# Optimization experiments

Hardware: AMD Instinct MI355X
Metric: run time of the kernel (lower is better)

## Reference

```python
import jax, jax.numpy as jnp
import numpy as np

NL, DM, DI, DS, DC, DR, NC = 4, 128, 256, 16, 4, 8, 10
ALPHA = 0.3  # observer_alpha

def layernorm(x, w, b, eps=1e-5):
    m = x.mean(-1, keepdims=True)
    v = ((x - m) ** 2).mean(-1, keepdims=True)
    return (x - m) / jnp.sqrt(v + eps) * w + b

def silu(x):
    return x * jax.nn.sigmoid(x)

def causal_dwconv(x, w, b):
    # x: (B, L, DI); w: (DI, 1, DC); b: (DI,)
    xt = x.transpose(0, 2, 1)  # (B, DI, L)
    y = jax.lax.conv_general_dilated(
        xt, w, window_strides=(1,), padding=[(DC - 1, 0)],
        dimension_numbers=('NCH', 'OIH', 'NCH'), feature_group_count=DI)
    return (y + b[None, :, None]).transpose(0, 2, 1)  # (B, L, DI)

def ssm_scan(delta, Bc, Cc, u, A):
    # delta, u: (B, L, DI); Bc, Cc: (B, L, DS); A: (DI, DS)
    B = delta.shape[0]
    def step(h, inp):
        d_t, b_t, c_t, u_t = inp  # (B,DI),(B,DS),(B,DS),(B,DI)
        dA = jnp.exp(d_t[..., None] * A)              # (B, DI, DS)
        h = dA * h + (d_t * u_t)[..., None] * b_t[:, None, :]
        y = jnp.einsum('bds,bs->bd', h, c_t)
        return h, y
    h0 = jnp.zeros((B, DI, DS), delta.dtype)
    xs = (delta.transpose(1, 0, 2), Bc.transpose(1, 0, 2),
          Cc.transpose(1, 0, 2), u.transpose(1, 0, 2))
    _, ys = jax.lax.scan(step, h0, xs)
    return ys.transpose(1, 0, 2)  # (B, L, DI)

def _forward(x, W_in, b_in, ln_w, ln_b, in_proj_w, conv_w, conv_b, x_proj_w,
             dt_proj_w, dt_proj_b, A_log, Dp, out_proj_w, out_proj_b,
             norm_w, norm_b, cls_w, cls_b):
    B = x.shape[0]
    u = x.transpose(0, 2, 3, 1).reshape(B, -1, 3)   # (B, L, 3)
    h = u @ W_in + b_in                              # (B, L, DM)
    for i in range(NL):
        res = h
        z = layernorm(h, ln_w[i], ln_b[i])
        xz = z @ in_proj_w[i]                        # (B, L, 2*DI)
        xin, gate = jnp.split(xz, 2, axis=-1)
        xc = silu(causal_dwconv(xin, conv_w[i], conv_b[i]))  # (B, L, DI)
        proj = xc @ x_proj_w[i]                      # (B, L, DR + 2*DS)
        dt, Bc, Cc = jnp.split(proj, [DR, DR + DS], axis=-1)
        delta = jax.nn.softplus(dt @ dt_proj_w[i] + dt_proj_b[i])  # (B, L, DI)
        A = -jnp.exp(A_log[i])                       # (DI, DS)
        y = ssm_scan(delta, Bc, Cc, xc, A) + xc * Dp[i]
        # Luenberger-style observer correction: blend predicted SSM output
        y = (1.0 - ALPHA) * y + ALPHA * xc
        y = y * silu(gate)
        h = res + y @ out_proj_w[i] + out_proj_b[i]
    pooled = h.mean(axis=1)                          # (B, DM)
    pooled = layernorm(pooled, norm_w, norm_b)
    return pooled @ cls_w + cls_b                    # (B, NC)

def setup_inputs():
    key = jax.random.key(0)
    ks = jax.random.split(key, 8)
    def nrm(k, shape, std=0.02):
        return jax.random.normal(k, shape, jnp.float32) * std
    return {
        'x': jax.random.normal(ks[0], (32, 3, 32, 32), jnp.float32),
        'W_in': nrm(ks[1], (3, DM)), 'b_in': jnp.zeros((DM,), jnp.float32),
        'ln_w': jnp.ones((NL, DM), jnp.float32), 'ln_b': jnp.zeros((NL, DM), jnp.float32),
        'in_proj_w': nrm(ks[2], (NL, DM, 2 * DI)),
        'conv_w': nrm(ks[3], (NL, DI, 1, DC), 0.2), 'conv_b': jnp.zeros((NL, DI), jnp.float32),
        'x_proj_w': nrm(ks[4], (NL, DI, DR + 2 * DS)),
        'dt_proj_w': nrm(ks[5], (NL, DR, DI), 0.1),
        'dt_proj_b': jnp.full((NL, DI), -4.6, jnp.float32),
        'A_log': jnp.log(jnp.broadcast_to(jnp.arange(1, DS + 1, dtype=jnp.float32), (NL, DI, DS))),
        'Dp': jnp.ones((NL, DI), jnp.float32),
        'out_proj_w': nrm(ks[6], (NL, DI, DM)), 'out_proj_b': jnp.zeros((NL, DM), jnp.float32),
        'norm_w': jnp.ones((DM,), jnp.float32), 'norm_b': jnp.zeros((DM,), jnp.float32),
        'cls_w': nrm(ks[7], (DM, NC)), 'cls_b': jnp.zeros((NC,), jnp.float32),
    }

def reference(x, W_in, b_in, ln_w, ln_b, in_proj_w, conv_w, conv_b, x_proj_w,
              dt_proj_w, dt_proj_b, A_log, Dp, out_proj_w, out_proj_b,
              norm_w, norm_b, cls_w, cls_b):
    return _forward(x, W_in, b_in, ln_w, ln_b, in_proj_w, conv_w, conv_b,
                    x_proj_w, dt_proj_w, dt_proj_b, A_log, Dp, out_proj_w,
                    out_proj_b, norm_w, norm_b, cls_w, cls_b)
```

## Files before the change

### kernel.cpp

```cpp
#include <hip/hip_runtime.h>
#include <math.h>

#define B_  32
#define L_  1024
#define T_  (B_ * L_)
#define DM_ 128
#define DI_ 256
#define DS_ 16
#define DC_ 4
#define DR_ 8
#define NC_ 10
#define CHUNK_ 32
#define NCH_  (L_ / CHUNK_)
#define PSTR_ 64

typedef __bf16 bf16x8 __attribute__((ext_vector_type(8)));
typedef __bf16 bf16x4 __attribute__((ext_vector_type(4)));
typedef __bf16 bf16x2 __attribute__((ext_vector_type(2)));
typedef float f32x4 __attribute__((ext_vector_type(4)));

__device__ __forceinline__ float sigmoidf_(float x) { return 1.0f / (1.0f + __expf(-x)); }
__device__ __forceinline__ float siluf_(float x)    { return x * sigmoidf_(x); }
__device__ __forceinline__ float softplusf_(float x) {
    return (x > 15.0f) ? x : __logf(1.0f + __expf(x));
}
__device__ __forceinline__ float fexp2_(float x) { return __builtin_amdgcn_exp2f(x); }

__device__ __forceinline__ void gload_lds16(const __bf16* g, __bf16* l) {
    __builtin_amdgcn_global_load_lds(
        (const __attribute__((address_space(1))) void*)g,
        (__attribute__((address_space(3))) void*)l, 16, 0, 0);
}

template<int R>
__device__ __forceinline__ void stage_async(const __bf16* __restrict__ src,
        __bf16* lds, int k0, int stride, int wid, int lane) {
    constexpr int NI = R / 32;
#pragma unroll
    for (int j = 0; j < NI; ++j) {
        int s0 = (wid * NI + j) * 64;
        int s = s0 + lane;
        int row = s >> 3, sw = s & 7;
        int slot = sw ^ (row & 7);
        gload_lds16(src + (size_t)row * stride + k0 + slot * 8, lds + (size_t)s0 * 8);
    }
}

__global__ __launch_bounds__(128) void k_embed(const float* __restrict__ x,
        const float* __restrict__ Win, const float* __restrict__ bin,
        float* __restrict__ h) {
    int t = blockIdx.x;
    int b = t >> 10, l = t & 1023;
    int m = threadIdx.x;
    const float* xb = x + (size_t)b * 3 * 1024 + l;
    float acc = bin[m];
    acc = fmaf(xb[0],    Win[m],        acc);
    acc = fmaf(xb[1024], Win[128 + m],  acc);
    acc = fmaf(xb[2048], Win[256 + m],  acc);
    h[(size_t)t * 128 + m] = acc;
}

__global__ __launch_bounds__(256) void k_prep(const float* __restrict__ ipw,
        const float* __restrict__ opw, const float* __restrict__ xpw,
        __bf16* __restrict__ wt1, __bf16* __restrict__ wt2,
        __bf16* __restrict__ wcat) {
    int blk = blockIdx.x;
    int tid = threadIdx.x;
    int i = blk * 256 + tid;
    {
        int lay = i >> 16, rem = i & 65535, n = rem >> 7, k = rem & 127;
        wt1[i] = (__bf16)ipw[lay * 65536 + k * 512 + n];
    }
    if (i < 131072) {
        int lay = i >> 15, rem = i & 32767, n = rem >> 8, k = rem & 255;
        wt2[i] = (__bf16)opw[lay * 32768 + k * 128 + n];
    }
    if (blk < 256) {
        int lay = blk >> 6, n = blk & 63;
        int k = tid;
        float v = (n < 40) ? xpw[lay * 10240 + k * 40 + n] : 0.0f;
        wcat[(size_t)blk * 256 + k] = (__bf16)v;
    }
}

__global__ __launch_bounds__(256) void k_ln(const float* __restrict__ h,
        const float* __restrict__ w, const float* __restrict__ b,
        __bf16* __restrict__ z) {
    int wid = threadIdx.x >> 6, lane = threadIdx.x & 63;
    int t = blockIdx.x * 4 + wid;
    const float* hr = h + (size_t)t * 128;
    float2 v = *(const float2*)(hr + lane * 2);
    float s = v.x + v.y, sq = v.x * v.x + v.y * v.y;
#pragma unroll
    for (int off = 1; off < 64; off <<= 1) {
        s += __shfl_xor(s, off);
        sq += __shfl_xor(sq, off);
    }
    float mean = s * (1.0f / 128.0f);
    float var = sq * (1.0f / 128.0f) - mean * mean;
    float rstd = rsqrtf(var + 1e-5f);
    float2 wv = *(const float2*)(w + lane * 2);
    float2 bv = *(const float2*)(b + lane * 2);
    bf16x2 o;
    o.x = (__bf16)((v.x - mean) * rstd * wv.x + bv.x);
    o.y = (__bf16)((v.y - mean) * rstd * wv.y + bv.y);
    *(bf16x2*)(z + (size_t)t * 128 + lane * 2) = o;
}

template<int BM, int K, int N, int MODE, bool GATE, bool WLN>
__global__ __launch_bounds__(256) void k_gemm_mfma(
        const __bf16* __restrict__ A, const __bf16* __restrict__ G,
        const __bf16* __restrict__ Wt, const float* __restrict__ bias,
        float* __restrict__ Cf, __bf16* __restrict__ Cb,
        const float* __restrict__ lnw, const float* __restrict__ lnb,
        __bf16* __restrict__ Zb) {
    static_assert(!GATE || BM == 32, "GATE staging assumes BM=32");
    static_assert(!WLN || (MODE == 2 && BM == 32 && N == 128), "WLN geometry");
    __shared__ __bf16 As[BM * 64];
    __shared__ __bf16 Bs[128 * 64];
    __shared__ float red_s[WLN ? 4 : 1][WLN ? 32 : 1];
    __shared__ float red_q[WLN ? 4 : 1][WLN ? 32 : 1];
    int tid = threadIdx.x;
    int bm = blockIdx.x, bn = blockIdx.y;
    int lane = tid & 63, wid = tid >> 6;
    int lr = lane & 15, lg = lane >> 4;
    constexpr int MF = BM / 16;

    f32x4 acc[MF][2] = {};
    const __bf16* Asrc = A + (size_t)(bm * BM) * K;
    const __bf16* Bsrc = Wt + (size_t)(bn * 128) * K;

    for (int k0 = 0; k0 < K; k0 += 64) {
        if (GATE) {
            int row = tid >> 3, slot = tid & 7;
            int m = bm * BM + row;
            bf16x8 yv = *(const bf16x8*)(A + (size_t)m * K + k0 + slot * 8);
            bf16x8 gv = *(const bf16x8*)(G + (size_t)m * 256 + k0 + slot * 8);
            bf16x8 v;
#pragma unroll
            for (int j = 0; j < 8; ++j)
                v[j] = (__bf16)((float)yv[j] * (float)gv[j]);
            *(bf16x8*)(As + row * 64 + ((slot ^ (row & 7)) * 8)) = v;
        } else {
            stage_async<BM>(Asrc, As, k0, K, wid, lane);
        }
        stage_async<128>(Bsrc, Bs, k0, K, wid, lane);
        __syncthreads();
#pragma unroll
        for (int ks = 0; ks < 2; ++ks) {
            int slotbase = ks * 4 + lg;
            bf16x8 af[MF], bfr[2];
#pragma unroll
            for (int m = 0; m < MF; ++m) {
                int row = m * 16 + lr;
                af[m] = *(const bf16x8*)(As + row * 64 + ((slotbase ^ (row & 7)) * 8));
            }
#pragma unroll
            for (int n = 0; n < 2; ++n) {
                int rn = wid * 32 + n * 16 + lr;
                bfr[n] = *(const bf16x8*)(Bs + rn * 64 + ((slotbase ^ (rn & 7)) * 8));
            }
#pragma unroll
            for (int m = 0; m < MF; ++m)
#pragma unroll
                for (int n = 0; n < 2; ++n)
                    acc[m][n] = __builtin_amdgcn_mfma_f32_16x16x32_bf16(
                        af[m], bfr[n], acc[m][n], 0, 0, 0);
        }
        __syncthreads();
    }
    float vv[MF][2][4];
#pragma unroll
    for (int m = 0; m < MF; ++m) {
#pragma unroll
        for (int n = 0; n < 2; ++n) {
            int col = bn * 128 + wid * 32 + n * 16 + lr;
            float bv = (MODE == 2) ? bias[col] : 0.0f;
#pragma unroll
            for (int rg = 0; rg < 4; ++rg) {
                int row = bm * BM + m * 16 + lg * 4 + rg;
                float v = acc[m][n][rg];
                if (MODE == 0) {
                    if (col < 256)
                        Cb[(size_t)row * 256 + col] = (__bf16)v;
                    else
                        Zb[(size_t)row * 256 + (col - 256)] = (__bf16)siluf_(v);
                } else if (MODE == 1) {
                    if (col < 40)
                        Cb[(size_t)row * PSTR_ + col] = (__bf16)v;
                } else {
                    float* cp = Cf + (size_t)row * N + col;
                    v += *cp + bv;
                    *cp = v;
                    vv[m][n][rg] = v;
                }
            }
        }
    }
    if (WLN) {
        float ps[MF][4], pq[MF][4];
#pragma unroll
        for (int m = 0; m < MF; ++m)
#pragma unroll
            for (int rg = 0; rg < 4; ++rg) {
                float a = vv[m][0][rg], bv2 = vv[m][1][rg];
                ps[m][rg] = a + bv2;
                pq[m][rg] = a * a + bv2 * bv2;
            }
#pragma unroll
        for (int off = 1; off < 16; off <<= 1) {
#pragma unroll
            for (int m = 0; m < MF; ++m)
#pragma unroll
                for (int rg = 0; rg < 4; ++rg) {
                    ps[m][rg] += __shfl_xor(ps[m][rg], off);
                    pq[m][rg] += __shfl_xor(pq[m][rg], off);
                }
        }
        if (lr == 0) {
#pragma unroll
            for (int m = 0; m < MF; ++m)
#pragma unroll
                for (int rg = 0; rg < 4; ++rg) {
                    int rl = m * 16 + lg * 4 + rg;
                    red_s[wid][rl] = ps[m][rg];
                    red_q[wid][rl] = pq[m][rg];
                }
        }
        __syncthreads();
#pragma unroll
        for (int m = 0; m < MF; ++m)
#pragma unroll
            for (int rg = 0; rg < 4; ++rg) {
                int rl = m * 16 + lg * 4 + rg;
                float s = red_s[0][rl] + red_s[1][rl] + red_s[2][rl] + red_s[3][rl];
                float q = red_q[0][rl] + red_q[1][rl] + red_q[2][rl] + red_q[3][rl];
                float mean = s * (1.0f / 128.0f);
                float var = q * (1.0f / 128.0f) - mean * mean;
                float rstd = rsqrtf(var + 1e-5f);
#pragma unroll
                for (int n = 0; n < 2; ++n) {
                    int col = wid * 32 + n * 16 + lr;
                    float z = (vv[m][n][rg] - mean) * rstd * lnw[col] + lnb[col];
                    Zb[(size_t)(bm * BM + rl) * 128 + col] = (__bf16)z;
                }
            }
    }
}

__global__ __launch_bounds__(256) void k_conv(const __bf16* __restrict__ xinb,
        const float* __restrict__ cw, const float* __restrict__ cb,
        __bf16* __restrict__ xcb) {
    int t = blockIdx.x * 4 + (threadIdx.x >> 6);
    int d0 = (threadIdx.x & 63) * 4;
    int l = t & 1023;
    const __bf16* xp = xinb + (size_t)t * 256 + d0;
    float4 wv[4];
#pragma unroll
    for (int j = 0; j < 4; ++j) wv[j] = *(const float4*)(cw + (d0 + j) * 4);
    float acc[4] = {cb[d0], cb[d0 + 1], cb[d0 + 2], cb[d0 + 3]};
#pragma unroll
    for (int k = 0; k < 4; ++k) {
        int back = 3 - k;
        if (l >= back) {
            bf16x4 v = *(const bf16x4*)(xp - back * 256);
#pragma unroll
            for (int j = 0; j < 4; ++j)
                acc[j] = fmaf((float)v[j], ((const float*)&wv[j])[k], acc[j]);
        }
    }
    bf16x4 o;
#pragma unroll
    for (int j = 0; j < 4; ++j) o[j] = (__bf16)siluf_(acc[j]);
    *(bf16x4*)(xcb + (size_t)t * 256 + d0) = o;
}

template<bool FINAL>
__global__ __launch_bounds__(128) void k_scan_chunk(
        const __bf16* __restrict__ projall, const __bf16* __restrict__ xcb,
        const float* __restrict__ dtw, const float* __restrict__ dtb,
        const float* __restrict__ Alog, const float* __restrict__ Dp,
        float* __restrict__ P, float* __restrict__ S,
        __bf16* __restrict__ yb) {
    __shared__ __bf16 xcs[CHUNK_ * 128];
    __shared__ float bc[CHUNK_ * 32];
    __shared__ float dts[CHUNK_ * 8];
    int b = blockIdx.z, c = blockIdx.y, dg = blockIdx.x;
    int tid = threadIdx.x;
    int d = dg * 128 + tid;

    const __bf16* projC = projall + ((size_t)b * 1024 + c * CHUNK_) * PSTR_;
    const __bf16* xcC   = xcb + ((size_t)b * 1024 + c * CHUNK_) * 256 + dg * 128;

#pragma unroll
    for (int r = 0; r < (CHUNK_ * 16) / 128; ++r) {
        int item = r * 128 + tid;
        int t = item >> 4, o8 = (item & 15) * 8;
        *(bf16x8*)(xcs + t * 128 + o8) = *(const bf16x8*)(xcC + (size_t)t * 256 + o8);
    }
    {
        int t = tid >> 2, g8 = (tid & 3) * 8;
        bf16x8 v = *(const bf16x8*)(projC + (size_t)t * PSTR_ + 8 + g8);
        float4 f0 = {(float)v[0], (float)v[1], (float)v[2], (float)v[3]};
        float4 f1 = {(float)v[4], (float)v[5], (float)v[6], (float)v[7]};
        *(float4*)(bc + t * 32 + g8)     = f0;
        *(float4*)(bc + t * 32 + g8 + 4) = f1;
    }
    if (tid < CHUNK_) {
        bf16x8 v = *(const bf16x8*)(projC + (size_t)tid * PSTR_);
#pragma unroll
        for (int j = 0; j < 8; ++j) dts[tid * 8 + j] = (float)v[j];
    }

    float dtwc[8];
#pragma unroll
    for (int r = 0; r < 8; ++r) dtwc[r] = dtw[r * 256 + d];
    float dtbd = dtb[d];
    float aa[16], hs[16];
#pragma unroll
    for (int jj = 0; jj < 4; ++jj) {
        float4 av = *(const float4*)(Alog + (size_t)d * 16 + jj * 4);
        aa[jj * 4 + 0] = -__expf(av.x) * 1.44269504088896f;
        aa[jj * 4 + 1] = -__expf(av.y) * 1.44269504088896f;
        aa[jj * 4 + 2] = -__expf(av.z) * 1.44269504088896f;
        aa[jj * 4 + 3] = -__expf(av.w) * 1.44269504088896f;
    }
    float Dpd = Dp[d];
    size_t psIdx = ((size_t)(b * NCH_ + c)) * 4096 + (size_t)d * 16;
    if (FINAL) {
#pragma unroll
        for (int jj = 0; jj < 4; ++jj) {
            float4 h0 = *(const float4*)(P + psIdx + jj * 4);
            hs[jj * 4 + 0] = h0.x; hs[jj * 4 + 1] = h0.y;
            hs[jj * 4 + 2] = h0.z; hs[jj * 4 + 3] = h0.w;
        }
    } else {
#pragma unroll
        for (int j = 0; j < 16; ++j) hs[j] = 0.0f;
    }
    float cumd = 0.0f;
    __bf16* yC = yb + ((size_t)b * 1024 + c * CHUNK_) * 256 + dg * 128 + tid;

    __syncthreads();
#pragma unroll 2
    for (int tt = 0; tt < CHUNK_; ++tt) {
        const float* dtr = dts + tt * 8;
        float4 dt0 = *(const float4*)(dtr);
        float4 dt1 = *(const float4*)(dtr + 4);
        float dtv = dtbd;
        dtv = fmaf(dt0.x, dtwc[0], dtv); dtv = fmaf(dt0.y, dtwc[1], dtv);
        dtv = fmaf(dt0.z, dtwc[2], dtv); dtv = fmaf(dt0.w, dtwc[3], dtv);
        dtv = fmaf(dt1.x, dtwc[4], dtv); dtv = fmaf(dt1.y, dtwc[5], dtv);
        dtv = fmaf(dt1.z, dtwc[6], dtv); dtv = fmaf(dt1.w, dtwc[7], dtv);
        float delta_t = softplusf_(dtv);
        float u = (float)xcs[tt * 128 + tid];
        float du = delta_t * u;
        const float* bcr = bc + tt * 32;
        if (!FINAL) cumd += delta_t;
        float ys = 0.0f;
#pragma unroll
        for (int jj = 0; jj < 4; ++jj) {
            float4 Bv = *(const float4*)(bcr + jj * 4);
            float4 Cv;
            if (FINAL) Cv = *(const float4*)(bcr + 16 + jj * 4);
#pragma unroll
            for (int j = 0; j < 4; ++j) {
                int s = jj * 4 + j;
                float dA = fexp2_(delta_t * aa[s]);
                hs[s] = fmaf(dA, hs[s], du * ((const float*)&Bv)[j]);
                if (FINAL) ys = fmaf(hs[s], ((const float*)&Cv)[j], ys);
            }
        }
        if (FINAL) {
            float yv = fmaf(u, Dpd, ys);
            yv = fmaf(0.7f, yv, 0.3f * u);
            yC[(size_t)tt * 256] = (__bf16)yv;
        }
    }
    if (!FINAL) {
#pragma unroll
        for (int jj = 0; jj < 4; ++jj) {
            float4 pv, sv;
            pv.x = fexp2_(aa[jj * 4 + 0] * cumd);
            pv.y = fexp2_(aa[jj * 4 + 1] * cumd);
            pv.z = fexp2_(aa[jj * 4 + 2] * cumd);
            pv.w = fexp2_(aa[jj * 4 + 3] * cumd);
            sv.x = hs[jj * 4 + 0]; sv.y = hs[jj * 4 + 1];
            sv.z = hs[jj * 4 + 2]; sv.w = hs[jj * 4 + 3];
            *(float4*)(P + psIdx + jj * 4) = pv;
            *(float4*)(S + psIdx + jj * 4) = sv;
        }
    }
}

__global__ __launch_bounds__(256) void k_scan_combine(float* __restrict__ P,
        const float* __restrict__ S) {
    int idx = blockIdx.x * 256 + threadIdx.x;
    int b = idx >> 12, rem = idx & 4095;
    float h = 0.0f;
#pragma unroll
    for (int c = 0; c < NCH_; ++c) {
        size_t base = ((size_t)(b * NCH_ + c)) * 4096 + rem;
        float p = P[base];
        float s = S[base];
        P[base] = h;
        h = fmaf(p, h, s);
    }
}

__global__ __launch_bounds__(128) void k_pool(const float* __restrict__ h,
        float* __restrict__ partial) {
    int b = blockIdx.x, lc = blockIdx.y;
    int m = threadIdx.x;
    const float* hb = h + (size_t)b * 131072 + (size_t)lc * 128 * 128 + m;
    float acc = 0.0f;
#pragma unroll 8
    for (int l = 0; l < 128; ++l) acc += hb[(size_t)l * 128];
    partial[((size_t)b * 8 + lc) * 128 + m] = acc;
}

__global__ __launch_bounds__(128) void k_head(const float* __restrict__ partial,
        const float* __restrict__ nw, const float* __restrict__ nb,
        const float* __restrict__ cw, const float* __restrict__ cb,
        float* __restrict__ out) {
    __shared__ float zs[128];
    __shared__ float red[128];
    int b = blockIdx.x, m = threadIdx.x;
    float v = 0.0f;
#pragma unroll
    for (int lc = 0; lc < 8; ++lc) v += partial[((size_t)b * 8 + lc) * 128 + m];
    v *= (1.0f / 1024.0f);
    red[m] = v;
    __syncthreads();
    for (int off = 64; off; off >>= 1) {
        if (m < off) red[m] += red[m + off];
        __syncthreads();
    }
    float mean = red[0] * (1.0f / 128.0f);
    __syncthreads();
    float dv = v - mean;
    red[m] = dv * dv;
    __syncthreads();
    for (int off = 64; off; off >>= 1) {
        if (m < off) red[m] += red[m + off];
        __syncthreads();
    }
    float rstd = rsqrtf(red[0] * (1.0f / 128.0f) + 1e-5f);
    zs[m] = dv * rstd * nw[m] + nb[m];
    __syncthreads();
    if (m < NC_) {
        float acc = cb[m];
#pragma unroll 8
        for (int k = 0; k < 128; ++k) acc = fmaf(zs[k], cw[k * 10 + m], acc);
        out[b * 10 + m] = acc;
    }
}

extern "C" void kernel_launch(void* const* d_in, const int* in_sizes, int n_in,
                              void* d_out, int out_size, void* d_ws, size_t ws_size,
                              hipStream_t stream) {
    const float* x    = (const float*)d_in[0];
    const float* Win  = (const float*)d_in[1];
    const float* bin  = (const float*)d_in[2];
    const float* lnw  = (const float*)d_in[3];
    const float* lnb  = (const float*)d_in[4];
    const float* ipw  = (const float*)d_in[5];
    const float* cw   = (const float*)d_in[6];
    const float* cb   = (const float*)d_in[7];
    const float* xpw  = (const float*)d_in[8];
    const float* dtw  = (const float*)d_in[9];
    const float* dtb  = (const float*)d_in[10];
    const float* Alog = (const float*)d_in[11];
    const float* Dp   = (const float*)d_in[12];
    const float* opw  = (const float*)d_in[13];
    const float* opb  = (const float*)d_in[14];
    const float* nw   = (const float*)d_in[15];
    const float* nb   = (const float*)d_in[16];
    const float* clw  = (const float*)d_in[17];
    const float* clb  = (const float*)d_in[18];

    float* ws = (float*)d_ws;
    float*  h       = ws;
    float*  P       = ws + 4194304;
    __bf16* zb      = (__bf16*)(ws + 4194304);
    __bf16* xinb    = (__bf16*)(ws + 8388608);
    __bf16* sgb     = (__bf16*)(ws + 12582912);
    __bf16* xcb     = (__bf16*)(ws + 16777216);
    __bf16* projall = (__bf16*)(ws + 20971520);
    __bf16* yb      = (__bf16*)(ws + 25690112);
    float*  partial = ws + 29884416;
    __bf16* wt1     = (__bf16*)(ws + 29917184);
    __bf16* wt2     = (__bf16*)(ws + 30048256);
    __bf16* wcat    = (__bf16*)(ws + 30113792);
    float*  Sb      = ws + 30310400;

    k_prep<<<1024, 256, 0, stream>>>(ipw, opw, xpw, wt1, wt2, wcat);
    k_embed<<<T_, 128, 0, stream>>>(x, Win, bin, h);
    k_ln<<<T_ / 4, 256, 0, stream>>>(h, lnw, lnb, zb);
    for (int lay = 0; lay < 4; ++lay) {
        k_gemm_mfma<64, 128, 512, 0, false, false><<<dim3(T_ / 64, 4), 256, 0, stream>>>(
            zb, nullptr, wt1 + (size_t)lay * 65536, nullptr, nullptr, xinb,
            nullptr, nullptr, sgb);
        k_conv<<<T_ / 4, 256, 0, stream>>>(xinb, cw + lay * 1024, cb + lay * 256, xcb);
        k_gemm_mfma<64, 256, 128, 1, false, false><<<dim3(T_ / 64, 1), 256, 0, stream>>>(
            xcb, nullptr, wcat + (size_t)lay * 16384, nullptr, nullptr, projall,
            nullptr, nullptr, nullptr);
        k_scan_chunk<false><<<dim3(2, NCH_, B_), 128, 0, stream>>>(projall, xcb,
            dtw + lay * 2048, dtb + lay * 256, Alog + lay * 4096, Dp + lay * 256,
            P, Sb, yb);
        k_scan_combine<<<B_ * 4096 / 256, 256, 0, stream>>>(P, Sb);
        k_scan_chunk<true><<<dim3(2, NCH_, B_), 128, 0, stream>>>(projall, xcb,
            dtw + lay * 2048, dtb + lay * 256, Alog + lay * 4096, Dp + lay * 256,
            P, Sb, yb);
        if (lay < 3) {
            k_gemm_mfma<32, 256, 128, 2, true, true><<<dim3(T_ / 32, 1), 256, 0, stream>>>(
                yb, sgb, wt2 + (size_t)lay * 32768, opb + lay * 128, h, nullptr,
                lnw + (lay + 1) * 128, lnb + (lay + 1) * 128, zb);
        } else {
            k_gemm_mfma<32, 256, 128, 2, true, false><<<dim3(T_ / 32, 1), 256, 0, stream>>>(
                yb, sgb, wt2 + (size_t)lay * 32768, opb + lay * 128, h, nullptr,
                nullptr, nullptr, nullptr);
        }
    }
    k_pool<<<dim3(32, 8), 128, 0, stream>>>(h, partial);
    k_head<<<32, 128, 0, stream>>>(partial, nw, nb, clw, clb, (float*)d_out);
}
```

Before: 621.2 us.

## Fuse embed+LN, conv+x_proj, and mean-pool into neighbouring kernels

Merges the embedding and first layernorm into one kernel, fuses the depthwise causal conv with the small x_proj projection (scalar FMA against LDS-staged weights) in one kernel, and folds the sequence mean-pool into the last out-proj GEMM epilogue so the head reads per-block partial sums. This removes several launches and the round trips of h and xcb through global memory. In exchange the x_proj product moves from MFMA to scalar FP32 FMA, which may cost more compute per token.

After: 749.6 us. 20.7% more time.

```diff
diff --git a/kernel.cpp b/kernel.cpp
--- a/kernel.cpp
+++ b/kernel.cpp
@@ -46,18 +46,35 @@
     }
 }
 
-__global__ __launch_bounds__(128) void k_embed(const float* __restrict__ x,
+__global__ __launch_bounds__(256) void k_embed_ln(const float* __restrict__ x,
         const float* __restrict__ Win, const float* __restrict__ bin,
-        float* __restrict__ h) {
-    int t = blockIdx.x;
+        const float* __restrict__ lnw, const float* __restrict__ lnb,
+        float* __restrict__ h, __bf16* __restrict__ z) {
+    int wid = threadIdx.x >> 6, lane = threadIdx.x & 63;
+    int t = blockIdx.x * 4 + wid;
     int b = t >> 10, l = t & 1023;
-    int m = threadIdx.x;
     const float* xb = x + (size_t)b * 3 * 1024 + l;
-    float acc = bin[m];
-    acc = fmaf(xb[0],    Win[m],        acc);
-    acc = fmaf(xb[1024], Win[128 + m],  acc);
-    acc = fmaf(xb[2048], Win[256 + m],  acc);
-    h[(size_t)t * 128 + m] = acc;
+    float x0 = xb[0], x1 = xb[1024], x2 = xb[2048];
+    int m = lane * 2;
+    float2 v;
+    v.x = bin[m]     + x0 * Win[m]     + x1 * Win[128 + m]     + x2 * Win[256 + m];
+    v.y = bin[m + 1] + x0 * Win[m + 1] + x1 * Win[128 + m + 1] + x2 * Win[256 + m + 1];
+    *(float2*)(h + (size_t)t * 128 + m) = v;
+    float s = v.x + v.y, sq = v.x * v.x + v.y * v.y;
+#pragma unroll
+    for (int off = 1; off < 64; off <<= 1) {
+        s += __shfl_xor(s, off);
+        sq += __shfl_xor(sq, off);
+    }
+    float mean = s * (1.0f / 128.0f);
+    float var = sq * (1.0f / 128.0f) - mean * mean;
+    float rstd = rsqrtf(var + 1e-5f);
+    float2 wv = *(const float2*)(lnw + m);
+    float2 bv = *(const float2*)(lnb + m);
+    bf16x2 o;
+    o.x = (__bf16)((v.x - mean) * rstd * wv.x + bv.x);
+    o.y = (__bf16)((v.y - mean) * rstd * wv.y + bv.y);
+    *(bf16x2*)(z + (size_t)t * 128 + m) = o;
 }
 
 __global__ __launch_bounds__(256) void k_prep(const float* __restrict__ ipw,
@@ -83,39 +100,16 @@
     }
 }
 
-__global__ __launch_bounds__(256) void k_ln(const float* __restrict__ h,
-        const float* __restrict__ w, const float* __restrict__ b,
-        __bf16* __restrict__ z) {
-    int wid = threadIdx.x >> 6, lane = threadIdx.x & 63;
-    int t = blockIdx.x * 4 + wid;
-    const float* hr = h + (size_t)t * 128;
-    float2 v = *(const float2*)(hr + lane * 2);
-    float s = v.x + v.y, sq = v.x * v.x + v.y * v.y;
-#pragma unroll
-    for (int off = 1; off < 64; off <<= 1) {
-        s += __shfl_xor(s, off);
-        sq += __shfl_xor(sq, off);
-    }
-    float mean = s * (1.0f / 128.0f);
-    float var = sq * (1.0f / 128.0f) - mean * mean;
-    float rstd = rsqrtf(var + 1e-5f);
-    float2 wv = *(const float2*)(w + lane * 2);
-    float2 bv = *(const float2*)(b + lane * 2);
-    bf16x2 o;
-    o.x = (__bf16)((v.x - mean) * rstd * wv.x + bv.x);
-    o.y = (__bf16)((v.y - mean) * rstd * wv.y + bv.y);
-    *(bf16x2*)(z + (size_t)t * 128 + lane * 2) = o;
-}
-
-template<int BM, int K, int N, int MODE, bool GATE, bool WLN>
+template<int BM, int K, int N, int MODE, bool GATE, bool WLN, bool POOL>
 __global__ __launch_bounds__(256) void k_gemm_mfma(
         const __bf16* __restrict__ A, const __bf16* __restrict__ G,
         const __bf16* __restrict__ Wt, const float* __restrict__ bias,
         float* __restrict__ Cf, __bf16* __restrict__ Cb,
         const float* __restrict__ lnw, const float* __restrict__ lnb,
-        __bf16* __restrict__ Zb) {
+        __bf16* __restrict__ Zb, float* __restrict__ Pool) {
     static_assert(!GATE || BM == 32, "GATE staging assumes BM=32");
     static_assert(!WLN || (MODE == 2 && BM == 32 && N == 128), "WLN geometry");
+    static_assert(!POOL || (MODE == 2 && BM == 32 && N == 128), "POOL geometry");
     __shared__ __bf16 As[BM * 64];
     __shared__ __bf16 Bs[128 * 64];
     __shared__ float red_s[WLN ? 4 : 1][WLN ? 32 : 1];
@@ -185,9 +179,6 @@
                         Cb[(size_t)row * 256 + col] = (__bf16)v;
                     else
                         Zb[(size_t)row * 256 + (col - 256)] = (__bf16)siluf_(v);
-                } else if (MODE == 1) {
-                    if (col < 40)
-                        Cb[(size_t)row * PSTR_ + col] = (__bf16)v;
                 } else {
                     float* cp = Cf + (size_t)row * N + col;
                     v += *cp + bv;
@@ -246,33 +237,98 @@
                 }
             }
     }
-}
-
-__global__ __launch_bounds__(256) void k_conv(const __bf16* __restrict__ xinb,
+    if (POOL) {
+#pragma unroll
+        for (int n = 0; n < 2; ++n) {
+            float s = 0.0f;
+#pragma unroll
+            for (int m = 0; m < MF; ++m)
+#pragma unroll
+                for (int rg = 0; rg < 4; ++rg) s += vv[m][n][rg];
+            s += __shfl_xor(s, 16);
+            s += __shfl_xor(s, 32);
+            if (lg == 0)
+                Pool[(size_t)bm * 128 + wid * 32 + n * 16 + lr] = s;
+        }
+    }
+}
+
+__global__ __launch_bounds__(256) void k_convproj(const __bf16* __restrict__ xinb,
         const float* __restrict__ cw, const float* __restrict__ cb,
-        __bf16* __restrict__ xcb) {
-    int t = blockIdx.x * 4 + (threadIdx.x >> 6);
-    int d0 = (threadIdx.x & 63) * 4;
+        const __bf16* __restrict__ wcat, __bf16* __restrict__ xcb,
+        __bf16* __restrict__ projall) {
+    __shared__ float xcs[16 * 257];
+    __shared__ __bf16 wlds[40 * 264];
+    int tid = threadIdx.x;
+    int t0 = blockIdx.x * 16;
+#pragma unroll
+    for (int r = 0; r < 5; ++r) {
+        int item = r * 256 + tid;
+        int n = item >> 5, g8 = (item & 31) * 8;
+        *(bf16x8*)(wlds + n * 264 + g8) = *(const bf16x8*)(wcat + n * 256 + g8);
+    }
+    int tl = tid >> 4, c0 = (tid & 15) * 16;
+    int t = t0 + tl;
     int l = t & 1023;
-    const __bf16* xp = xinb + (size_t)t * 256 + d0;
-    float4 wv[4];
-#pragma unroll
-    for (int j = 0; j < 4; ++j) wv[j] = *(const float4*)(cw + (d0 + j) * 4);
-    float acc[4] = {cb[d0], cb[d0 + 1], cb[d0 + 2], cb[d0 + 3]};
+    const __bf16* xp = xinb + (size_t)t * 256 + c0;
+    float accv[16];
+#pragma unroll
+    for (int j = 0; j < 16; ++j) accv[j] = cb[c0 + j];
 #pragma unroll
     for (int k = 0; k < 4; ++k) {
         int back = 3 - k;
         if (l >= back) {
-            bf16x4 v = *(const bf16x4*)(xp - back * 256);
-#pragma unroll
-            for (int j = 0; j < 4; ++j)
-                acc[j] = fmaf((float)v[j], ((const float*)&wv[j])[k], acc[j]);
-        }
-    }
-    bf16x4 o;
-#pragma unroll
-    for (int j = 0; j < 4; ++j) o[j] = (__bf16)siluf_(acc[j]);
-    *(bf16x4*)(xcb + (size_t)t * 256 + d0) = o;
+            bf16x8 v0 = *(const bf16x8*)(xp - back * 256);
+            bf16x8 v1 = *(const bf16x8*)(xp - back * 256 + 8);
+#pragma unroll
+            for (int j = 0; j < 8; ++j) {
+                accv[j]     = fmaf((float)v0[j], cw[(c0 + j) * 4 + k], accv[j]);
+                accv[8 + j] = fmaf((float)v1[j], cw[(c0 + 8 + j) * 4 + k], accv[8 + j]);
+            }
+        }
+    }
+    bf16x8 o0, o1;
+#pragma unroll
+    for (int j = 0; j < 8; ++j) {
+        float v = siluf_(accv[j]);
+        o0[j] = (__bf16)v; xcs[tl * 257 + c0 + j] = v;
+    }
+#pragma unroll
+    for (int j = 0; j < 8; ++j) {
+        float v = siluf_(accv[8 + j]);
+        o1[j] = (__bf16)v; xcs[tl * 257 + c0 + 8 + j] = v;
+    }
+    *(bf16x8*)(xcb + (size_t)t * 256 + c0)     = o0;
+    *(bf16x8*)(xcb + (size_t)t * 256 + c0 + 8) = o1;
+    __syncthreads();
+    int q = tid & 15;
+    bool has2 = q < 8;
+    float acc0 = 0.0f, acc1 = 0.0f, acc2 = 0.0f;
+    const __bf16* w0 = wlds + q * 264;
+    const __bf16* w1 = wlds + (q + 16) * 264;
+    const __bf16* w2 = wlds + (q + 32) * 264;
+#pragma unroll 4
+    for (int k8 = 0; k8 < 256; k8 += 8) {
+        float xv[8];
+#pragma unroll
+        for (int j = 0; j < 8; ++j) xv[j] = xcs[tl * 257 + k8 + j];
+        bf16x8 a = *(const bf16x8*)(w0 + k8);
+        bf16x8 b = *(const bf16x8*)(w1 + k8);
+#pragma unroll
+        for (int j = 0; j < 8; ++j) {
+            acc0 = fmaf(xv[j], (float)a[j], acc0);
+            acc1 = fmaf(xv[j], (float)b[j], acc1);
+        }
+        if (has2) {
+            bf16x8 c2 = *(const bf16x8*)(w2 + k8);
+#pragma unroll
+            for (int j = 0; j < 8; ++j) acc2 = fmaf(xv[j], (float)c2[j], acc2);
+        }
+    }
+    __bf16* pr = projall + (size_t)t * PSTR_;
+    pr[q] = (__bf16)acc0;
+    pr[q + 16] = (__bf16)acc1;
+    if (has2) pr[q + 32] = (__bf16)acc2;
 }
 
 template<bool FINAL>
@@ -408,18 +464,7 @@
     }
 }
 
-__global__ __launch_bounds__(128) void k_pool(const float* __restrict__ h,
-        float* __restrict__ partial) {
-    int b = blockIdx.x, lc = blockIdx.y;
-    int m = threadIdx.x;
-    const float* hb = h + (size_t)b * 131072 + (size_t)lc * 128 * 128 + m;
-    float acc = 0.0f;
-#pragma unroll 8
-    for (int l = 0; l < 128; ++l) acc += hb[(size_t)l * 128];
-    partial[((size_t)b * 8 + lc) * 128 + m] = acc;
-}
-
-__global__ __launch_bounds__(128) void k_head(const float* __restrict__ partial,
+__global__ __launch_bounds__(128) void k_head(const float* __restrict__ pool2,
         const float* __restrict__ nw, const float* __restrict__ nb,
         const float* __restrict__ cw, const float* __restrict__ cb,
         float* __restrict__ out) {
@@ -427,8 +472,8 @@
     __shared__ float red[128];
     int b = blockIdx.x, m = threadIdx.x;
     float v = 0.0f;
-#pragma unroll
-    for (int lc = 0; lc < 8; ++lc) v += partial[((size_t)b * 8 + lc) * 128 + m];
+#pragma unroll 8
+    for (int i = 0; i < 32; ++i) v += pool2[(size_t)(b * 32 + i) * 128 + m];
     v *= (1.0f / 1024.0f);
     red[m] = v;
     __syncthreads();
@@ -488,23 +533,20 @@
     __bf16* xcb     = (__bf16*)(ws + 16777216);
     __bf16* projall = (__bf16*)(ws + 20971520);
     __bf16* yb      = (__bf16*)(ws + 25690112);
-    float*  partial = ws + 29884416;
     __bf16* wt1     = (__bf16*)(ws + 29917184);
     __bf16* wt2     = (__bf16*)(ws + 30048256);
     __bf16* wcat    = (__bf16*)(ws + 30113792);
     float*  Sb      = ws + 30310400;
+    float*  pool2   = ws + 34504704;
 
     k_prep<<<1024, 256, 0, stream>>>(ipw, opw, xpw, wt1, wt2, wcat);
-    k_embed<<<T_, 128, 0, stream>>>(x, Win, bin, h);
-    k_ln<<<T_ / 4, 256, 0, stream>>>(h, lnw, lnb, zb);
+    k_embed_ln<<<T_ / 4, 256, 0, stream>>>(x, Win, bin, lnw, lnb, h, zb);
     for (int lay = 0; lay < 4; ++lay) {
-        k_gemm_mfma<64, 128, 512, 0, false, false><<<dim3(T_ / 64, 4), 256, 0, stream>>>(
+        k_gemm_mfma<64, 128, 512, 0, false, false, false><<<dim3(T_ / 64, 4), 256, 0, stream>>>(
             zb, nullptr, wt1 + (size_t)lay * 65536, nullptr, nullptr, xinb,
-            nullptr, nullptr, sgb);
-        k_conv<<<T_ / 4, 256, 0, stream>>>(xinb, cw + lay * 1024, cb + lay * 256, xcb);
-        k_gemm_mfma<64, 256, 128, 1, false, false><<<dim3(T_ / 64, 1), 256, 0, stream>>>(
-            xcb, nullptr, wcat + (size_t)lay * 16384, nullptr, nullptr, projall,
-            nullptr, nullptr, nullptr);
+            nullptr, nullptr, sgb, nullptr);
+        k_convproj<<<T_ / 16, 256, 0, stream>>>(xinb, cw + lay * 1024, cb + lay * 256,
+            wcat + (size_t)lay * 16384, xcb, projall);
         k_scan_chunk<false><<<dim3(2, NCH_, B_), 128, 0, stream>>>(projall, xcb,
             dtw + lay * 2048, dtb + lay * 256, Alog + lay * 4096, Dp + lay * 256,
             P, Sb, yb);
@@ -513,15 +555,14 @@
             dtw + lay * 2048, dtb + lay * 256, Alog + lay * 4096, Dp + lay * 256,
             P, Sb, yb);
         if (lay < 3) {
-            k_gemm_mfma<32, 256, 128, 2, true, true><<<dim3(T_ / 32, 1), 256, 0, stream>>>(
+            k_gemm_mfma<32, 256, 128, 2, true, true, false><<<dim3(T_ / 32, 1), 256, 0, stream>>>(
                 yb, sgb, wt2 + (size_t)lay * 32768, opb + lay * 128, h, nullptr,
-                lnw + (lay + 1) * 128, lnb + (lay + 1) * 128, zb);
+                lnw + (lay + 1) * 128, lnb + (lay + 1) * 128, zb, nullptr);
         } else {
-            k_gemm_mfma<32, 256, 128, 2, true, false><<<dim3(T_ / 32, 1), 256, 0, stream>>>(
+            k_gemm_mfma<32, 256, 128, 2, true, false, true><<<dim3(T_ / 32, 1), 256, 0, stream>>>(
                 yb, sgb, wt2 + (size_t)lay * 32768, opb + lay * 128, h, nullptr,
-                nullptr, nullptr, nullptr);
-        }
-    }
-    k_pool<<<dim3(32, 8), 128, 0, stream>>>(h, partial);
-    k_head<<<32, 128, 0, stream>>>(partial, nw, nb, clw, clb, (float*)d_out);
-}
+                nullptr, nullptr, nullptr, pool2);
+        }
+    }
+    k_head<<<32, 128, 0, stream>>>(pool2, nw, nb, clw, clb, (float*)d_out);
+}
```
